# Kernel optimization log

Hardware: AMD Instinct MI355X
Metric: run time of the kernel (lower is better)

The kernel has to match this reference:

```python
import jax, jax.numpy as jnp
import numpy as np

B, C, F, T = 8, 2, 1024, 1024
NB, BW, EMB = 64, 16, 128
FEAT = C * BW * 2  # in_channels * bandwidth * reim = 64
EPS = 1e-5


def setup_inputs() -> dict:
    key = jax.random.key(0)
    k1, k2, k3, k4 = jax.random.split(key, 4)
    bound = 1.0 / np.sqrt(FEAT)
    return {
        "x_real": jax.random.normal(k1, (B, C, F, T), dtype=jnp.float32),
        "x_imag": jax.random.normal(k2, (B, C, F, T), dtype=jnp.float32),
        "ln_w": jnp.ones((NB, FEAT), dtype=jnp.float32),
        "ln_b": jnp.zeros((NB, FEAT), dtype=jnp.float32),
        "fc_w": jax.random.uniform(k3, (NB, FEAT, EMB), dtype=jnp.float32, minval=-bound, maxval=bound),
        "fc_b": jax.random.uniform(k4, (NB, EMB), dtype=jnp.float32, minval=-bound, maxval=bound),
    }


def reference(x_real, x_imag, ln_w, ln_b, fc_w, fc_b):
    b, c, f, t = x_real.shape
    nb, feat = ln_w.shape
    bw = f // nb
    # permute (B,C,F,T) -> (B,T,C,F), split F into (nb, bw)
    xr = jnp.transpose(x_real, (0, 3, 1, 2)).reshape(b, t, c, nb, bw)
    xi = jnp.transpose(x_imag, (0, 3, 1, 2)).reshape(b, t, c, nb, bw)
    # view_as_real ordering: feature axis is (C, bw, reim)
    xb = jnp.stack([xr, xi], axis=-1)                 # (B,T,C,nb,bw,2)
    xb = jnp.transpose(xb, (0, 3, 1, 2, 4, 5))        # (B,nb,T,C,bw,2)
    xb = xb.reshape(b, nb, t, feat)                   # (B,nb,T,feat)
    # per-band LayerNorm over last axis
    mean = jnp.mean(xb, axis=-1, keepdims=True)
    var = jnp.mean(jnp.square(xb - mean), axis=-1, keepdims=True)
    xn = (xb - mean) * jax.lax.rsqrt(var + EPS)
    xn = xn * ln_w[None, :, None, :] + ln_b[None, :, None, :]
    # per-band Linear: grouped GEMM over bands
    z = jnp.einsum('bntf,nfe->bnte', xn, fc_w) + fc_b[None, :, None, :]
    return z  # (B, n_bands, T, emb_dim)
```

## Files before the change

### kernel.cpp

```cpp
#include <hip/hip_runtime.h>

#define Bdim   8
#define Cdim   2
#define Fdim   1024
#define Tdim   1024
#define NB     64
#define BWb    16
#define EMB    128
#define FEAT   64
#define TILE_T 64
#define NTHR   256
#define EPSV   1e-5f

__global__ __launch_bounds__(NTHR, 3) void bandsplit_kernel(
    const float* __restrict__ xr, const float* __restrict__ xi,
    const float* __restrict__ lnw, const float* __restrict__ lnb,
    const float* __restrict__ fcw, const float* __restrict__ fcb,
    float* __restrict__ out)
{
    __shared__ float xs[FEAT][TILE_T];
    __shared__ float wt[FEAT][EMB];
    __shared__ float sb[EMB];
    __shared__ float slnw[FEAT];
    __shared__ float slnb[FEAT];
    __shared__ float smu[TILE_T];
    __shared__ float srs[TILE_T];

    const int tid = threadIdx.x;
    const int bid = blockIdx.x;
    const int tb  = bid & 15;
    const int n   = (bid >> 4) & 63;
    const int b   = bid >> 10;
    const int t0g = tb * TILE_T;

    {
        const float4* wsrc = (const float4*)(fcw + (size_t)n * FEAT * EMB);
        float4* wdst = (float4*)&wt[0][0];
#pragma unroll
        for (int k = 0; k < 8; ++k)
            wdst[tid + k * NTHR] = wsrc[tid + k * NTHR];

        if (tid < EMB)            sb[tid]         = fcb[n * EMB + tid];
        else if (tid < EMB + 64)  slnw[tid - EMB] = lnw[n * FEAT + (tid - EMB)];
        else if (tid < EMB + 128) slnb[tid - EMB - 64] = lnb[n * FEAT + (tid - EMB - 64)];
    }

#pragma unroll
    for (int k = 0; k < 4; ++k) {
        const int v  = tid + k * NTHR;
        const int f  = v >> 4;
        const int tq = v & 15;
        const int c  = f >> 5;
        const int w  = (f >> 1) & 15;
        const float* src = ((f & 1) ? xi : xr)
            + (((size_t)(b * Cdim + c) * Fdim + (n * BWb + w)) * Tdim + t0g + tq * 4);
        *(float4*)&xs[f][tq * 4] = *(const float4*)src;
    }
    __syncthreads();

    {
        const int t = tid >> 2;
        const int p = tid & 3;
        float s = 0.f, ss = 0.f;
#pragma unroll
        for (int j = 0; j < 16; ++j) {
            const float v = xs[p * 16 + j][t];
            s += v; ss += v * v;
        }
        s += __shfl_xor(s, 1); ss += __shfl_xor(ss, 1);
        s += __shfl_xor(s, 2); ss += __shfl_xor(ss, 2);
        if (p == 0) {
            const float mu  = s * (1.f / 64.f);
            const float var = ss * (1.f / 64.f) - mu * mu;
            smu[t] = mu;
            srs[t] = rsqrtf(var + EPSV);
        }
    }
    __syncthreads();

#pragma unroll
    for (int k = 0; k < 4; ++k) {
        const int v  = tid + k * NTHR;
        const int f  = v >> 4;
        const int tq = v & 15;
        float4 x  = *(float4*)&xs[f][tq * 4];
        const float4 mu = *(const float4*)&smu[tq * 4];
        const float4 rs = *(const float4*)&srs[tq * 4];
        const float gw = slnw[f], gb = slnb[f];
        x.x = (x.x - mu.x) * rs.x * gw + gb;
        x.y = (x.y - mu.y) * rs.y * gw + gb;
        x.z = (x.z - mu.z) * rs.z * gw + gb;
        x.w = (x.w - mu.w) * rs.w * gw + gb;
        *(float4*)&xs[f][tq * 4] = x;
    }
    __syncthreads();

    const int t0 = (tid >> 4) * 4;
    const int e0 = (tid & 15) * 8;

    float acc[4][8];
#pragma unroll
    for (int i = 0; i < 4; ++i)
#pragma unroll
        for (int j = 0; j < 8; ++j) acc[i][j] = 0.f;

#pragma unroll 4
    for (int f = 0; f < FEAT; ++f) {
        const float4 av = *(const float4*)&xs[f][t0];
        const float4 b0 = *(const float4*)&wt[f][e0];
        const float4 b1 = *(const float4*)&wt[f][e0 + 4];
        const float a[4]  = {av.x, av.y, av.z, av.w};
        const float bb[8] = {b0.x, b0.y, b0.z, b0.w, b1.x, b1.y, b1.z, b1.w};
#pragma unroll
        for (int i = 0; i < 4; ++i)
#pragma unroll
            for (int j = 0; j < 8; ++j)
                acc[i][j] = fmaf(a[i], bb[j], acc[i][j]);
    }

    const float4 bias0 = *(const float4*)&sb[e0];
    const float4 bias1 = *(const float4*)&sb[e0 + 4];
    const size_t obase = (((size_t)(b * NB + n)) * Tdim + (t0g + t0)) * EMB + e0;
#pragma unroll
    for (int i = 0; i < 4; ++i) {
        float4 o0, o1;
        o0.x = acc[i][0] + bias0.x; o0.y = acc[i][1] + bias0.y;
        o0.z = acc[i][2] + bias0.z; o0.w = acc[i][3] + bias0.w;
        o1.x = acc[i][4] + bias1.x; o1.y = acc[i][5] + bias1.y;
        o1.z = acc[i][6] + bias1.z; o1.w = acc[i][7] + bias1.w;
        *(float4*)(out + obase + (size_t)i * EMB)     = o0;
        *(float4*)(out + obase + (size_t)i * EMB + 4) = o1;
    }
}

extern "C" void kernel_launch(void* const* d_in, const int* in_sizes, int n_in,
                              void* d_out, int out_size, void* d_ws, size_t ws_size,
                              hipStream_t stream) {
    const float* xr  = (const float*)d_in[0];
    const float* xi  = (const float*)d_in[1];
    const float* lnw = (const float*)d_in[2];
    const float* lnb = (const float*)d_in[3];
    const float* fcw = (const float*)d_in[4];
    const float* fcb = (const float*)d_in[5];
    float* out = (float*)d_out;

    const int grid = Bdim * NB * (Tdim / TILE_T);
    hipLaunchKernelGGL(bandsplit_kernel, dim3(grid), dim3(NTHR), 0, stream,
                       xr, xi, lnw, lnb, fcw, fcb, out);
}
```

Before: 405.5 us.

## Use split-bf16 MFMA for per-band GEMM with swizzled LDS operands

```diff
diff --git a/kernel.cpp b/kernel.cpp
--- a/kernel.cpp
+++ b/kernel.cpp
@@ -12,38 +12,42 @@
 #define NTHR   256
 #define EPSV   1e-5f
 
+typedef __attribute__((ext_vector_type(8))) short bf16x8;
+typedef __attribute__((ext_vector_type(4))) float f32x4;
+
+__device__ __forceinline__ unsigned short f2bf(float x) {
+    union { float f; unsigned u; } v; v.f = x;
+    const unsigned r = v.u + 0x7FFFu + ((v.u >> 16) & 1u);
+    return (unsigned short)(r >> 16);
+}
+__device__ __forceinline__ float bf2f(unsigned short b) {
+    union { float f; unsigned u; } v; v.u = ((unsigned)b) << 16;
+    return v.f;
+}
+
 __global__ __launch_bounds__(NTHR, 3) void bandsplit_kernel(
     const float* __restrict__ xr, const float* __restrict__ xi,
     const float* __restrict__ lnw, const float* __restrict__ lnb,
     const float* __restrict__ fcw, const float* __restrict__ fcb,
     float* __restrict__ out)
 {
-    __shared__ float xs[FEAT][TILE_T];
-    __shared__ float wt[FEAT][EMB];
+    __shared__ __align__(16) float xs[FEAT][TILE_T];
+    __shared__ __align__(16) unsigned short w_hi[EMB][FEAT];
+    __shared__ __align__(16) unsigned short w_lo[EMB][FEAT];
     __shared__ float sb[EMB];
     __shared__ float slnw[FEAT];
     __shared__ float slnb[FEAT];
     __shared__ float smu[TILE_T];
     __shared__ float srs[TILE_T];
 
-    const int tid = threadIdx.x;
-    const int bid = blockIdx.x;
-    const int tb  = bid & 15;
-    const int n   = (bid >> 4) & 63;
-    const int b   = bid >> 10;
-    const int t0g = tb * TILE_T;
-
-    {
-        const float4* wsrc = (const float4*)(fcw + (size_t)n * FEAT * EMB);
-        float4* wdst = (float4*)&wt[0][0];
-#pragma unroll
-        for (int k = 0; k < 8; ++k)
-            wdst[tid + k * NTHR] = wsrc[tid + k * NTHR];
-
-        if (tid < EMB)            sb[tid]         = fcb[n * EMB + tid];
-        else if (tid < EMB + 64)  slnw[tid - EMB] = lnw[n * FEAT + (tid - EMB)];
-        else if (tid < EMB + 128) slnb[tid - EMB - 64] = lnb[n * FEAT + (tid - EMB - 64)];
-    }
+    const int tid  = threadIdx.x;
+    const int lane = tid & 63;
+    const int wav  = tid >> 6;
+    const int bid  = blockIdx.x;
+    const int tb   = bid & 15;
+    const int n    = (bid >> 4) & 63;
+    const int b    = bid >> 10;
+    const int t0g  = tb * TILE_T;
 
 #pragma unroll
     for (int k = 0; k < 4; ++k) {
@@ -56,6 +60,39 @@
             + (((size_t)(b * Cdim + c) * Fdim + (n * BWb + w)) * Tdim + t0g + tq * 4);
         *(float4*)&xs[f][tq * 4] = *(const float4*)src;
     }
+
+    if (tid < EMB)            sb[tid]              = fcb[n * EMB + tid];
+    else if (tid < EMB + 64)  slnw[tid - EMB]      = lnw[n * FEAT + (tid - EMB)];
+    else if (tid < EMB + 128) slnb[tid - EMB - 64] = lnb[n * FEAT + (tid - EMB - 64)];
+
+    {
+        const int e  = tid & 127;
+        const int fh = (tid >> 7) * 32;
+        const float* wsrc = fcw + (size_t)n * FEAT * EMB + e;
+        float wv[32];
+#pragma unroll
+        for (int i = 0; i < 32; ++i)
+            wv[i] = wsrc[(size_t)(fh + i) * EMB];
+
+        char* const whb = (char*)&w_hi[0][0] + e * 128;
+        char* const wlb = (char*)&w_lo[0][0] + e * 128;
+#pragma unroll
+        for (int cc = 0; cc < 4; ++cc) {
+            unsigned hw[4], lw[4];
+#pragma unroll
+            for (int j = 0; j < 4; ++j) {
+                const float x0 = wv[cc * 8 + 2 * j];
+                const float x1 = wv[cc * 8 + 2 * j + 1];
+                const unsigned short h0 = f2bf(x0), h1 = f2bf(x1);
+                hw[j] = (unsigned)h0 | ((unsigned)h1 << 16);
+                lw[j] = (unsigned)f2bf(x0 - bf2f(h0))
+                      | ((unsigned)f2bf(x1 - bf2f(h1)) << 16);
+            }
+            const int cs = ((fh >> 3) + cc) ^ (e & 7);
+            *(uint4*)(whb + cs * 16) = make_uint4(hw[0], hw[1], hw[2], hw[3]);
+            *(uint4*)(wlb + cs * 16) = make_uint4(lw[0], lw[1], lw[2], lw[3]);
+        }
+    }
     __syncthreads();
 
     {
@@ -78,58 +115,85 @@
     }
     __syncthreads();
 
-#pragma unroll
-    for (int k = 0; k < 4; ++k) {
-        const int v  = tid + k * NTHR;
-        const int f  = v >> 4;
-        const int tq = v & 15;
-        float4 x  = *(float4*)&xs[f][tq * 4];
-        const float4 mu = *(const float4*)&smu[tq * 4];
-        const float4 rs = *(const float4*)&srs[tq * 4];
-        const float gw = slnw[f], gb = slnb[f];
-        x.x = (x.x - mu.x) * rs.x * gw + gb;
-        x.y = (x.y - mu.y) * rs.y * gw + gb;
-        x.z = (x.z - mu.z) * rs.z * gw + gb;
-        x.w = (x.w - mu.w) * rs.w * gw + gb;
-        *(float4*)&xs[f][tq * 4] = x;
-    }
-    __syncthreads();
-
-    const int t0 = (tid >> 4) * 4;
-    const int e0 = (tid & 15) * 8;
-
-    float acc[4][8];
-#pragma unroll
-    for (int i = 0; i < 4; ++i)
-#pragma unroll
-        for (int j = 0; j < 8; ++j) acc[i][j] = 0.f;
-
-#pragma unroll 4
-    for (int f = 0; f < FEAT; ++f) {
-        const float4 av = *(const float4*)&xs[f][t0];
-        const float4 b0 = *(const float4*)&wt[f][e0];
-        const float4 b1 = *(const float4*)&wt[f][e0 + 4];
-        const float a[4]  = {av.x, av.y, av.z, av.w};
-        const float bb[8] = {b0.x, b0.y, b0.z, b0.w, b1.x, b1.y, b1.z, b1.w};
-#pragma unroll
-        for (int i = 0; i < 4; ++i)
-#pragma unroll
-            for (int j = 0; j < 8; ++j)
-                acc[i][j] = fmaf(a[i], bb[j], acc[i][j]);
-    }
-
-    const float4 bias0 = *(const float4*)&sb[e0];
-    const float4 bias1 = *(const float4*)&sb[e0 + 4];
-    const size_t obase = (((size_t)(b * NB + n)) * Tdim + (t0g + t0)) * EMB + e0;
-#pragma unroll
-    for (int i = 0; i < 4; ++i) {
-        float4 o0, o1;
-        o0.x = acc[i][0] + bias0.x; o0.y = acc[i][1] + bias0.y;
-        o0.z = acc[i][2] + bias0.z; o0.w = acc[i][3] + bias0.w;
-        o1.x = acc[i][4] + bias1.x; o1.y = acc[i][5] + bias1.y;
-        o1.z = acc[i][6] + bias1.z; o1.w = acc[i][7] + bias1.w;
-        *(float4*)(out + obase + (size_t)i * EMB)     = o0;
-        *(float4*)(out + obase + (size_t)i * EMB + 4) = o1;
+    uint4 hq[2], lq[2];
+    {
+        const int t = lane;
+        const float mu = smu[t], rs = srs[t];
+#pragma unroll
+        for (int u = 0; u < 2; ++u) {
+            const int fc = wav + u * 4;
+            float xv[8];
+#pragma unroll
+            for (int j = 0; j < 8; ++j) xv[j] = xs[fc * 8 + j][t];
+            unsigned hw[4], lw[4];
+#pragma unroll
+            for (int j = 0; j < 4; ++j) {
+                const int f0 = fc * 8 + 2 * j;
+                const float xn0 = (xv[2 * j]     - mu) * rs * slnw[f0]     + slnb[f0];
+                const float xn1 = (xv[2 * j + 1] - mu) * rs * slnw[f0 + 1] + slnb[f0 + 1];
+                const unsigned short h0 = f2bf(xn0), h1 = f2bf(xn1);
+                hw[j] = (unsigned)h0 | ((unsigned)h1 << 16);
+                lw[j] = (unsigned)f2bf(xn0 - bf2f(h0))
+                      | ((unsigned)f2bf(xn1 - bf2f(h1)) << 16);
+            }
+            hq[u] = make_uint4(hw[0], hw[1], hw[2], hw[3]);
+            lq[u] = make_uint4(lw[0], lw[1], lw[2], lw[3]);
+        }
+    }
+    __syncthreads();
+
+    {
+        char* const ab = (char*)&xs[0][0];
+        const int t = lane;
+#pragma unroll
+        for (int u = 0; u < 2; ++u) {
+            const int fc = wav + u * 4;
+            const int cs = fc ^ (t & 7);
+            *(uint4*)(ab +        t * 128 + cs * 16) = hq[u];
+            *(uint4*)(ab + 8192 + t * 128 + cs * 16) = lq[u];
+        }
+    }
+    __syncthreads();
+
+    const int lr   = lane & 15;
+    const int lh   = lane >> 4;
+    const int trow = wav * 16;
+
+    f32x4 acc[8];
+    const f32x4 zero = {0.f, 0.f, 0.f, 0.f};
+#pragma unroll
+    for (int et = 0; et < 8; ++et) acc[et] = zero;
+
+    const char* const ab  = (const char*)&xs[0][0];
+    const char* const whb = (const char*)&w_hi[0][0];
+    const char* const wlb = (const char*)&w_lo[0][0];
+
+#pragma unroll
+    for (int ks = 0; ks < 2; ++ks) {
+        const int ta = trow + lr;
+        const int ca = (ks * 4 + lh) ^ (ta & 7);
+        const bf16x8 ahf = *(const bf16x8*)(ab +        ta * 128 + ca * 16);
+        const bf16x8 alf = *(const bf16x8*)(ab + 8192 + ta * 128 + ca * 16);
+#pragma unroll
+        for (int et = 0; et < 8; ++et) {
+            const int er = et * 16 + lr;
+            const int cw = (ks * 4 + lh) ^ (er & 7);
+            const bf16x8 whf = *(const bf16x8*)(whb + er * 128 + cw * 16);
+            const bf16x8 wlf = *(const bf16x8*)(wlb + er * 128 + cw * 16);
+            acc[et] = __builtin_amdgcn_mfma_f32_16x16x32_bf16(ahf, whf, acc[et], 0, 0, 0);
+            acc[et] = __builtin_amdgcn_mfma_f32_16x16x32_bf16(ahf, wlf, acc[et], 0, 0, 0);
+            acc[et] = __builtin_amdgcn_mfma_f32_16x16x32_bf16(alf, whf, acc[et], 0, 0, 0);
+        }
+    }
+
+    const size_t obase = ((size_t)(b * NB + n) * Tdim + (t0g + trow + lh * 4)) * EMB;
+#pragma unroll
+    for (int et = 0; et < 8; ++et) {
+        const int   ec = et * 16 + lr;
+        const float be = sb[ec];
+#pragma unroll
+        for (int r = 0; r < 4; ++r)
+            out[obase + (size_t)r * EMB + ec] = acc[et][r] + be;
     }
 }
 
```

Result: faster. 376.7 us (-7.1%).
